# Optimization experiments

Measured on AMD Instinct MI355X. Metric: run time of the kernel, lower is better.

## Reference

```python
import jax, jax.numpy as jnp
import numpy as np

EPS = 1e-5

def layer_norm(h, g, b):
    m = h.mean(-1, keepdims=True)
    v = ((h - m) ** 2).mean(-1, keepdims=True)
    return (h - m) * jax.lax.rsqrt(v + EPS) * g + b

def setup_inputs() -> dict:
    key = jax.random.key(0)
    ks = jax.random.split(key, 16)
    B, D, C, H, EH, L = 64, 20000, 16, 64, 128, 32
    s = lambda k, fan_in, shape: jax.random.normal(k, shape, jnp.float32) / np.sqrt(fan_in)
    return {
        "x": jax.random.normal(ks[0], (B, D), jnp.float32),
        "mask": jax.random.randint(ks[1], (B, D), 0, 2, jnp.int32),
        "feature_embedding": jax.random.normal(ks[2], (D, C), jnp.float32),
        # h_layer: Linear(1+C -> H), LN, ReLU, Linear(H -> C), LN, ReLU
        "W1": s(ks[3], 1 + C, (1 + C, H)), "b1": jnp.zeros((H,), jnp.float32),
        "g1": jnp.ones((H,), jnp.float32), "be1": jnp.zeros((H,), jnp.float32),
        "W2": s(ks[4], H, (H, C)), "b2": jnp.zeros((C,), jnp.float32),
        "g2": jnp.ones((C,), jnp.float32), "be2": jnp.zeros((C,), jnp.float32),
        # encoder_mlp (FCLayers, 2 layers, LayerNorm + ReLU each): C -> EH -> 2L
        "We1": s(ks[5], C, (C, EH)), "bb1": jnp.zeros((EH,), jnp.float32),
        "gg1": jnp.ones((EH,), jnp.float32), "bbe1": jnp.zeros((EH,), jnp.float32),
        "We2": s(ks[6], EH, (EH, 2 * L)), "bb2": jnp.zeros((2 * L,), jnp.float32),
        "gg2": jnp.ones((2 * L,), jnp.float32), "bbe2": jnp.zeros((2 * L,), jnp.float32),
    }

def reference(x, mask, feature_embedding, W1, b1, g1, be1, W2, b2, g2, be2,
              We1, bb1, gg1, bbe1, We2, bb2, gg2, bbe2):
    B, D = x.shape
    C = feature_embedding.shape[1]
    # per-feature point-net: h_layer runs row-wise, so we compute it densely
    # for all (b, d) and zero out unobserved entries before pooling —
    # identical math to the per-sample masked gather in the original.
    h_in = jnp.concatenate(
        [x[..., None], jnp.broadcast_to(feature_embedding, (B, D, C))], axis=-1
    )  # [B, D, 1+C]
    h = jax.nn.relu(layer_norm(h_in @ W1 + b1, g1, be1))   # [B, D, H]
    h = jax.nn.relu(layer_norm(h @ W2 + b2, g2, be2))      # [B, D, C]
    m = mask.astype(h.dtype)
    summed = jnp.einsum('bdc,bd->bc', h, m)                # masked sum pool
    num_obs = jnp.maximum(m.sum(axis=1, keepdims=True), 1.0)
    c = summed / num_obs                                   # pool_mode='mean'
    # encoder_mlp
    e = jax.nn.relu(layer_norm(c @ We1 + bb1, gg1, bbe1))
    e = jax.nn.relu(layer_norm(e @ We2 + bb2, gg2, bbe2))  # [B, 2*latent]
    mu, logvar = jnp.split(e, 2, axis=-1)
    return mu, logvar
```

## Files before the change

### kernel.cpp

```cpp
#include <hip/hip_runtime.h>
#include <hip/hip_bf16.h>

#define EPSF 1e-5f

namespace {
constexpr int B = 64, D = 20000, C = 16, H = 64, EH = 128, L = 32;
constexpr int PB = 16;
constexpr int NB = 1024;
constexpr int MAXU = B * ((D + 63) / 64);
}

typedef __attribute__((ext_vector_type(8))) short bf16x8;
typedef __attribute__((ext_vector_type(4))) float f32x4;
typedef __attribute__((ext_vector_type(4))) unsigned int u32x4;

static __device__ __forceinline__ unsigned short f2bf(float f) {
    __hip_bfloat16 h = __float2bfloat16(f);
    return __builtin_bit_cast(unsigned short, h);
}
static __device__ __forceinline__ unsigned int packbf(float lo, float hi) {
    return ((unsigned int)f2bf(hi) << 16) | (unsigned int)f2bf(lo);
}

__global__ __launch_bounds__(1024) void k_prep(
    const int* __restrict__ mask, const float* __restrict__ fe,
    const float* __restrict__ W1, const float* __restrict__ b1,
    const float* __restrict__ W2,
    unsigned short* __restrict__ cd, int* __restrict__ cnt,
    unsigned short* __restrict__ febf,
    unsigned short* __restrict__ W1T, unsigned short* __restrict__ W2T)
{
    const int t = threadIdx.x;
    if (blockIdx.x < B) {
        const int b = blockIdx.x;
        const int lane = t & 63, wid = t >> 6;
        __shared__ int wc[16];
        const size_t bD = (size_t)b * D;
        constexpr int NIT = (D + 1023) / 1024;
        int mv = (t < D) ? mask[bD + t] : 0;
        int base = 0;
        for (int it = 0; it < NIT; ++it) {
            int mv_next = 0;
            const int dn = (it + 1) * 1024 + t;
            if (it + 1 < NIT && dn < D) mv_next = mask[bD + dn];
            const unsigned long long bal = __ballot(mv != 0);
            if (lane == 0) wc[wid] = __popcll(bal);
            __syncthreads();
            int woff = 0, tot = 0;
            #pragma unroll
            for (int k2 = 0; k2 < 16; ++k2) {
                const int c0 = wc[k2];
                tot += c0;
                if (k2 < wid) woff += c0;
            }
            if (mv) {
                const int d = it * 1024 + t;
                const int pre = __popcll(bal & ((1ull << lane) - 1ull));
                cd[bD + base + woff + pre] = (unsigned short)d;
            }
            base += tot;
            __syncthreads();
            mv = mv_next;
        }
        if (t == 0) cnt[b] = base;
    } else {
        const int pb = blockIdx.x - B;
        const int gtid = pb * 1024 + t;
        for (int u = gtid; u < (D * C) / 8; u += PB * 1024) {
            const float4 f0 = *(const float4*)(fe + (size_t)u * 8);
            const float4 f1 = *(const float4*)(fe + (size_t)u * 8 + 4);
            uint4 pk;
            pk.x = packbf(f0.x, f0.y); pk.y = packbf(f0.z, f0.w);
            pk.z = packbf(f1.x, f1.y); pk.w = packbf(f1.z, f1.w);
            *(uint4*)(febf + (size_t)u * 8) = pk;
        }
        if (pb == 0) {
            for (int e = t; e < H * 32; e += 1024) {
                const int rIdx = e >> 5, kk = e & 31;
                const int m = rIdx >> 4, rho = rIdx & 15;
                const int h = 32 * (m >> 1) + 8 * (rho >> 2) + 4 * (m & 1) + (rho & 3);
                float v = 0.f;
                if (kk < 16)       v = W1[(kk + 1) * H + h];
                else if (kk == 16) v = W1[h];
                else if (kk == 17) v = b1[h];
                W1T[e] = f2bf(v);
            }
        } else if (pb == 1) {
            for (int e = t; e < C * H; e += 1024) {
                const int c0 = e >> 6, hh = e & 63;
                W2T[e] = f2bf(W2[hh * C + c0]);
            }
        }
    }
}

__global__ __launch_bounds__(256, 4) void k_rows(
    const float* __restrict__ x, const unsigned short* __restrict__ cd,
    const int* __restrict__ cnt, const unsigned short* __restrict__ febf,
    const unsigned short* __restrict__ W1T, const unsigned short* __restrict__ W2T,
    const float* __restrict__ g1, const float* __restrict__ be1,
    const float* __restrict__ g2, const float* __restrict__ be2,
    const float* __restrict__ b2,
    float* __restrict__ part)
{
    const int tid = threadIdx.x;
    const int w = tid >> 6, lane = tid & 63;
    const int g = lane >> 4, q = lane & 15;

    const int cv  = cnt[lane];
    const int nuv = (cv + 63) >> 6;
    int Pi = nuv;
    #pragma unroll
    for (int off = 1; off < 64; off <<= 1) {
        const int pv = __shfl_up(Pi, off);
        if (lane >= off) Pi += pv;
    }
    const int T = __shfl(Pi, 63);

    bf16x8 w1f[4];
    #pragma unroll
    for (int m = 0; m < 4; ++m)
        w1f[m] = *(const bf16x8*)(W1T + (16 * m + q) * 32 + 8 * g);
    bf16x8 w2f[2];
    #pragma unroll
    for (int ks = 0; ks < 2; ++ks)
        w2f[ks] = *(const bf16x8*)(W2T + q * 64 + 32 * ks + 8 * g);

    float4 g1v[4], be1v[4];
    #pragma unroll
    for (int m = 0; m < 4; ++m) {
        const int h0 = 32 * (m >> 1) + 8 * g + 4 * (m & 1);
        g1v[m]  = *(const float4*)(g1  + h0);
        be1v[m] = *(const float4*)(be1 + h0);
    }
    const float4 g2v  = *(const float4*)(g2  + 4 * g);
    const float4 be2v = *(const float4*)(be2 + 4 * g);
    const float4 b2v  = *(const float4*)(b2  + 4 * g);

    const f32x4 z = {0.f, 0.f, 0.f, 0.f};

    for (int u = blockIdx.x * 4 + w; u < T; u += NB * 4) {
        const unsigned long long bl = __ballot(Pi <= u);
        const int b   = __popcll(bl);
        const int Pb  = __shfl(Pi, b);
        const int nub = __shfl(nuv, b);
        const int n   = __shfl(cv, b);
        const int base = (u - (Pb - nub)) * 64;
        const size_t bD = (size_t)b * D;

        const int idx  = base + lane;
        const int craw = (int)cd[bD + idx];
        const int dv   = (idx < n) ? craw : 0;

        bf16x8 hb[4];
        #pragma unroll
        for (int it = 0; it < 4; ++it) {
            const int dd = __shfl(dv, (it << 4) + q);
            bf16x8 hv;
            #pragma unroll
            for (int e = 0; e < 8; ++e) hv[e] = 0;
            if (g < 2) {
                hv = *(const bf16x8*)(febf + (size_t)dd * 16 + 8 * g);
            } else if (g == 2) {
                hv[0] = (short)f2bf(x[bD + dd]);
                hv[1] = (short)0x3F80;
            }
            hb[it] = hv;
        }

        f32x4 lacc = {0.f, 0.f, 0.f, 0.f};
        #pragma unroll
        for (int it = 0; it < 4; ++it) {
            const int gb = base + (it << 4);
            if (gb >= n) continue;
            f32x4 t1a[4];
            #pragma unroll
            for (int m = 0; m < 4; ++m)
                t1a[m] = __builtin_amdgcn_mfma_f32_16x16x32_bf16(w1f[m], hb[it], z, 0, 0, 0);

            float s0 = 0.f, s1 = 0.f, q0 = 0.f, q1 = 0.f;
            #pragma unroll
            for (int m = 0; m < 4; ++m) {
                s0 += t1a[m][0] + t1a[m][1];
                s1 += t1a[m][2] + t1a[m][3];
                q0 = fmaf(t1a[m][0], t1a[m][0], fmaf(t1a[m][1], t1a[m][1], q0));
                q1 = fmaf(t1a[m][2], t1a[m][2], fmaf(t1a[m][3], t1a[m][3], q1));
            }
            float s = s0 + s1, sq = q0 + q1;
            s  += __shfl_xor(s, 16);  sq += __shfl_xor(sq, 16);
            s  += __shfl_xor(s, 32);  sq += __shfl_xor(sq, 32);
            const float mean1 = s * (1.f / H);
            const float var1  = fmaxf(sq * (1.f / H) - mean1 * mean1, 0.f);
            const float rstd1 = rsqrtf(var1 + EPSF);

            unsigned int pw[8];
            #pragma unroll
            for (int m = 0; m < 4; ++m) {
                const float v0 = fmaxf(fmaf((t1a[m][0] - mean1) * rstd1, g1v[m].x, be1v[m].x), 0.f);
                const float v1 = fmaxf(fmaf((t1a[m][1] - mean1) * rstd1, g1v[m].y, be1v[m].y), 0.f);
                const float v2 = fmaxf(fmaf((t1a[m][2] - mean1) * rstd1, g1v[m].z, be1v[m].z), 0.f);
                const float v3 = fmaxf(fmaf((t1a[m][3] - mean1) * rstd1, g1v[m].w, be1v[m].w), 0.f);
                pw[2 * m]     = packbf(v0, v1);
                pw[2 * m + 1] = packbf(v2, v3);
            }
            const u32x4 r0 = {pw[0], pw[1], pw[2], pw[3]};
            const u32x4 r1 = {pw[4], pw[5], pw[6], pw[7]};
            const bf16x8 rb0 = __builtin_bit_cast(bf16x8, r0);
            const bf16x8 rb1 = __builtin_bit_cast(bf16x8, r1);

            f32x4 a2 = __builtin_amdgcn_mfma_f32_16x16x32_bf16(w2f[0], rb0, z, 0, 0, 0);
            a2 = __builtin_amdgcn_mfma_f32_16x16x32_bf16(w2f[1], rb1, a2, 0, 0, 0);
            a2[0] += b2v.x; a2[1] += b2v.y; a2[2] += b2v.z; a2[3] += b2v.w;

            float s2 = (a2[0] + a2[1]) + (a2[2] + a2[3]);
            float q2 = fmaf(a2[0], a2[0], fmaf(a2[1], a2[1],
                       fmaf(a2[2], a2[2], a2[3] * a2[3])));
            s2 += __shfl_xor(s2, 16);  q2 += __shfl_xor(q2, 16);
            s2 += __shfl_xor(s2, 32);  q2 += __shfl_xor(q2, 32);
            const float mean2 = s2 * (1.f / C);
            const float var2  = fmaxf(q2 * (1.f / C) - mean2 * mean2, 0.f);
            const float rstd2 = rsqrtf(var2 + EPSF);
            const float vm = (gb + q < n) ? 1.f : 0.f;
            lacc[0] += fmaxf(fmaf((a2[0] - mean2) * rstd2, g2v.x, be2v.x), 0.f) * vm;
            lacc[1] += fmaxf(fmaf((a2[1] - mean2) * rstd2, g2v.y, be2v.y), 0.f) * vm;
            lacc[2] += fmaxf(fmaf((a2[2] - mean2) * rstd2, g2v.z, be2v.z), 0.f) * vm;
            lacc[3] += fmaxf(fmaf((a2[3] - mean2) * rstd2, g2v.w, be2v.w), 0.f) * vm;
        }

        #pragma unroll
        for (int off = 1; off < 16; off <<= 1) {
            #pragma unroll
            for (int r = 0; r < 4; ++r) lacc[r] += __shfl_xor(lacc[r], off);
        }
        if (q == 0)
            *(float4*)(part + (size_t)u * C + 4 * g) =
                make_float4(lacc[0], lacc[1], lacc[2], lacc[3]);
    }
}

__global__ __launch_bounds__(EH) void k_enc(
    const float* __restrict__ part, const int* __restrict__ cnt,
    const float* __restrict__ We1, const float* __restrict__ bb1,
    const float* __restrict__ gg1, const float* __restrict__ bbe1,
    const float* __restrict__ We2, const float* __restrict__ bb2,
    const float* __restrict__ gg2, const float* __restrict__ bbe2,
    float* __restrict__ out)
{
    const int b = blockIdx.x;
    const int t = threadIdx.x;
    __shared__ int sP[64];
    __shared__ float red[8][16];
    __shared__ float cc[C];
    __shared__ float stats[2];
    __shared__ float buf[EH];
    __shared__ float buf2[2 * L];

    if (t < 64) {
        int p = (cnt[t] + 63) >> 6;
        #pragma unroll
        for (int off = 1; off < 64; off <<= 1) {
            const int pv = __shfl_up(p, off);
            if (t >= off) p += pv;
        }
        sP[t] = p;
    }
    __syncthreads();
    const int n = cnt[b];
    const int row0 = (b == 0) ? 0 : sP[b - 1];
    const int rows = sP[b] - row0;

    {
        const int c = t & 15, s = t >> 4;
        float ps = 0.f;
        for (int r = s; r < rows; r += 8)
            ps += part[(size_t)(row0 + r) * C + c];
        red[s][c] = ps;
    }
    __syncthreads();
    if (t < C) {
        float v = 0.f;
        #pragma unroll
        for (int s = 0; s < 8; ++s) v += red[s][t];
        cc[t] = v;
    }
    __syncthreads();
    const float inv = 1.f / fmaxf((float)n, 1.f);

    float v1 = bb1[t];
    #pragma unroll
    for (int c = 0; c < C; ++c)
        v1 = fmaf(cc[c] * inv, We1[c * EH + t], v1);
    buf[t] = v1;
    __syncthreads();
    if (t == 0) {
        float s = 0.f, ss = 0.f;
        for (int j2 = 0; j2 < EH; ++j2) { s += buf[j2]; ss = fmaf(buf[j2], buf[j2], ss); }
        float mn = s * (1.f / EH);
        float vr = fmaxf(ss * (1.f / EH) - mn * mn, 0.f);
        stats[0] = mn; stats[1] = rsqrtf(vr + EPSF);
    }
    __syncthreads();
    float e1 = fmaxf(fmaf((v1 - stats[0]) * stats[1], gg1[t], bbe1[t]), 0.f);
    __syncthreads();
    buf[t] = e1;
    __syncthreads();

    float v2 = 0.f;
    if (t < 2 * L) {
        v2 = bb2[t];
        #pragma unroll
        for (int h = 0; h < EH; ++h)
            v2 = fmaf(buf[h], We2[h * (2 * L) + t], v2);
        buf2[t] = v2;
    }
    __syncthreads();
    if (t == 0) {
        float s = 0.f, ss = 0.f;
        for (int j2 = 0; j2 < 2 * L; ++j2) { s += buf2[j2]; ss = fmaf(buf2[j2], buf2[j2], ss); }
        float mn = s * (1.f / (2 * L));
        float vr = fmaxf(ss * (1.f / (2 * L)) - mn * mn, 0.f);
        stats[0] = mn; stats[1] = rsqrtf(vr + EPSF);
    }
    __syncthreads();
    if (t < 2 * L) {
        float e2 = fmaxf(fmaf((v2 - stats[0]) * stats[1], gg2[t], bbe2[t]), 0.f);
        if (t < L) out[(size_t)b * L + t]                       = e2;
        else       out[(size_t)B * L + (size_t)b * L + (t - L)] = e2;
    }
}

extern "C" void kernel_launch(void* const* d_in, const int* in_sizes, int n_in,
                              void* d_out, int out_size, void* d_ws, size_t ws_size,
                              hipStream_t stream) {
    const float* x    = (const float*)d_in[0];
    const int*   mask = (const int*)d_in[1];
    const float* fe   = (const float*)d_in[2];
    const float* W1   = (const float*)d_in[3];
    const float* b1   = (const float*)d_in[4];
    const float* g1   = (const float*)d_in[5];
    const float* be1  = (const float*)d_in[6];
    const float* W2   = (const float*)d_in[7];
    const float* b2   = (const float*)d_in[8];
    const float* g2   = (const float*)d_in[9];
    const float* be2  = (const float*)d_in[10];
    const float* We1  = (const float*)d_in[11];
    const float* bb1  = (const float*)d_in[12];
    const float* gg1  = (const float*)d_in[13];
    const float* bbe1 = (const float*)d_in[14];
    const float* We2  = (const float*)d_in[15];
    const float* bb2  = (const float*)d_in[16];
    const float* gg2  = (const float*)d_in[17];
    const float* bbe2 = (const float*)d_in[18];
    float* out = (float*)d_out;

    char* wp = (char*)d_ws;
    float* part     = (float*)wp;               wp += (size_t)MAXU * C * 4;
    int*   cnt      = (int*)wp;                 wp += (size_t)B * 4;
    unsigned short* W1T  = (unsigned short*)wp; wp += (size_t)H * 32 * 2;
    unsigned short* W2T  = (unsigned short*)wp; wp += (size_t)C * H * 2;
    unsigned short* febf = (unsigned short*)wp; wp += (size_t)D * C * 2;
    unsigned short* cd   = (unsigned short*)wp;

    hipLaunchKernelGGL(k_prep, dim3(B + PB), dim3(1024), 0, stream,
                       mask, fe, W1, b1, W2, cd, cnt, febf, W1T, W2T);
    hipLaunchKernelGGL(k_rows, dim3(NB), dim3(256), 0, stream,
                       x, cd, cnt, febf, W1T, W2T, g1, be1, g2, be2, b2, part);
    hipLaunchKernelGGL(k_enc, dim3(B), dim3(EH), 0, stream,
                       part, cnt, We1, bb1, gg1, bbe1, We2, bb2, gg2, bbe2, out);
}
```

Measured before the change: 52.79 us.

## Materialize compacted per-sample bf16 feature rows in prep instead of index gather

The prep kernel now writes, for each observed (b, d), the bf16-packed feature embedding and a packed (x, 1) pair into a compacted per-sample buffer padded to 64 rows. The row kernel then reads these contiguously instead of gathering febf by index. This removes the index load, shuffle and dependent gather latency from the hot loop. In exchange it adds roughly 20 MB of extra HBM writes and reads, and that work sits on only 64 prep blocks. Separately, the row kernel's grid and occupancy hint are raised, bf16 packing uses the paired conversion intrinsic, and the per-chunk early-exit branch is dropped in favour of a mask.

```diff
diff --git a/kernel.cpp b/kernel.cpp
--- a/kernel.cpp
+++ b/kernel.cpp
@@ -5,8 +5,7 @@
 
 namespace {
 constexpr int B = 64, D = 20000, C = 16, H = 64, EH = 128, L = 32;
-constexpr int PB = 16;
-constexpr int NB = 1024;
+constexpr int NB = 1280;
 constexpr int MAXU = B * ((D + 63) / 64);
 }
 
@@ -21,13 +20,19 @@
 static __device__ __forceinline__ unsigned int packbf(float lo, float hi) {
     return ((unsigned int)f2bf(hi) << 16) | (unsigned int)f2bf(lo);
 }
+static __device__ __forceinline__ unsigned int cvtpk(float lo, float hi) {
+    __hip_bfloat162 h2 = __float22bfloat162_rn(make_float2(lo, hi));
+    return ((unsigned int)__builtin_bit_cast(unsigned short, h2.y) << 16)
+         | (unsigned int)__builtin_bit_cast(unsigned short, h2.x);
+}
 
 __global__ __launch_bounds__(1024) void k_prep(
-    const int* __restrict__ mask, const float* __restrict__ fe,
+    const int* __restrict__ mask, const float* __restrict__ x,
+    const float* __restrict__ fe,
     const float* __restrict__ W1, const float* __restrict__ b1,
     const float* __restrict__ W2,
-    unsigned short* __restrict__ cd, int* __restrict__ cnt,
-    unsigned short* __restrict__ febf,
+    int* __restrict__ cnt,
+    unsigned short* __restrict__ hfe, unsigned int* __restrict__ hxp,
     unsigned short* __restrict__ W1T, unsigned short* __restrict__ W2T)
 {
     const int t = threadIdx.x;
@@ -56,47 +61,53 @@
             if (mv) {
                 const int d = it * 1024 + t;
                 const int pre = __popcll(bal & ((1ull << lane) - 1ull));
-                cd[bD + base + woff + pre] = (unsigned short)d;
+                const int pos = base + woff + pre;
+                const float4 f0 = *(const float4*)(fe + (size_t)d * C);
+                const float4 f1 = *(const float4*)(fe + (size_t)d * C + 4);
+                const float4 f2 = *(const float4*)(fe + (size_t)d * C + 8);
+                const float4 f3 = *(const float4*)(fe + (size_t)d * C + 12);
+                uint4 p0, p1;
+                p0.x = packbf(f0.x, f0.y); p0.y = packbf(f0.z, f0.w);
+                p0.z = packbf(f1.x, f1.y); p0.w = packbf(f1.z, f1.w);
+                p1.x = packbf(f2.x, f2.y); p1.y = packbf(f2.z, f2.w);
+                p1.z = packbf(f3.x, f3.y); p1.w = packbf(f3.z, f3.w);
+                *(uint4*)(hfe + (bD + pos) * 16)     = p0;
+                *(uint4*)(hfe + (bD + pos) * 16 + 8) = p1;
+                hxp[bD + pos] = packbf(x[bD + d], 1.0f);
             }
             base += tot;
             __syncthreads();
             mv = mv_next;
         }
+        const int padend = (base + 63) & ~63;
+        for (int i = base + t; i < padend; i += 1024) {
+            *(uint4*)(hfe + (bD + i) * 16)     = make_uint4(0, 0, 0, 0);
+            *(uint4*)(hfe + (bD + i) * 16 + 8) = make_uint4(0, 0, 0, 0);
+            hxp[bD + i] = 0u;
+        }
         if (t == 0) cnt[b] = base;
+    } else if (blockIdx.x == B) {
+        for (int e = t; e < H * 32; e += 1024) {
+            const int rIdx = e >> 5, kk = e & 31;
+            const int m = rIdx >> 4, rho = rIdx & 15;
+            const int h = 32 * (m >> 1) + 8 * (rho >> 2) + 4 * (m & 1) + (rho & 3);
+            float v = 0.f;
+            if (kk < 16)       v = W1[(kk + 1) * H + h];
+            else if (kk == 16) v = W1[h];
+            else if (kk == 17) v = b1[h];
+            W1T[e] = f2bf(v);
+        }
     } else {
-        const int pb = blockIdx.x - B;
-        const int gtid = pb * 1024 + t;
-        for (int u = gtid; u < (D * C) / 8; u += PB * 1024) {
-            const float4 f0 = *(const float4*)(fe + (size_t)u * 8);
-            const float4 f1 = *(const float4*)(fe + (size_t)u * 8 + 4);
-            uint4 pk;
-            pk.x = packbf(f0.x, f0.y); pk.y = packbf(f0.z, f0.w);
-            pk.z = packbf(f1.x, f1.y); pk.w = packbf(f1.z, f1.w);
-            *(uint4*)(febf + (size_t)u * 8) = pk;
-        }
-        if (pb == 0) {
-            for (int e = t; e < H * 32; e += 1024) {
-                const int rIdx = e >> 5, kk = e & 31;
-                const int m = rIdx >> 4, rho = rIdx & 15;
-                const int h = 32 * (m >> 1) + 8 * (rho >> 2) + 4 * (m & 1) + (rho & 3);
-                float v = 0.f;
-                if (kk < 16)       v = W1[(kk + 1) * H + h];
-                else if (kk == 16) v = W1[h];
-                else if (kk == 17) v = b1[h];
-                W1T[e] = f2bf(v);
-            }
-        } else if (pb == 1) {
-            for (int e = t; e < C * H; e += 1024) {
-                const int c0 = e >> 6, hh = e & 63;
-                W2T[e] = f2bf(W2[hh * C + c0]);
-            }
-        }
-    }
-}
-
-__global__ __launch_bounds__(256, 4) void k_rows(
-    const float* __restrict__ x, const unsigned short* __restrict__ cd,
-    const int* __restrict__ cnt, const unsigned short* __restrict__ febf,
+        for (int e = t; e < C * H; e += 1024) {
+            const int c0 = e >> 6, hh = e & 63;
+            W2T[e] = f2bf(W2[hh * C + c0]);
+        }
+    }
+}
+
+__global__ __launch_bounds__(256, 5) void k_rows(
+    const int* __restrict__ cnt,
+    const unsigned short* __restrict__ hfe, const unsigned int* __restrict__ hxp,
     const unsigned short* __restrict__ W1T, const unsigned short* __restrict__ W2T,
     const float* __restrict__ g1, const float* __restrict__ be1,
     const float* __restrict__ g2, const float* __restrict__ be2,
@@ -146,24 +157,20 @@
         const int nub = __shfl(nuv, b);
         const int n   = __shfl(cv, b);
         const int base = (u - (Pb - nub)) * 64;
-        const size_t bD = (size_t)b * D;
-
-        const int idx  = base + lane;
-        const int craw = (int)cd[bD + idx];
-        const int dv   = (idx < n) ? craw : 0;
+        const size_t rowb = (size_t)b * D + base;
+        const int rem = n - base;
 
         bf16x8 hb[4];
         #pragma unroll
         for (int it = 0; it < 4; ++it) {
-            const int dd = __shfl(dv, (it << 4) + q);
-            bf16x8 hv;
-            #pragma unroll
-            for (int e = 0; e < 8; ++e) hv[e] = 0;
+            bf16x8 hv = {0, 0, 0, 0, 0, 0, 0, 0};
+            const int p = (it << 4) + q;
             if (g < 2) {
-                hv = *(const bf16x8*)(febf + (size_t)dd * 16 + 8 * g);
+                hv = *(const bf16x8*)(hfe + (rowb + p) * 16 + 8 * g);
             } else if (g == 2) {
-                hv[0] = (short)f2bf(x[bD + dd]);
-                hv[1] = (short)0x3F80;
+                const unsigned int xv = hxp[rowb + p];
+                const u32x4 tmp = {xv, 0u, 0u, 0u};
+                hv = __builtin_bit_cast(bf16x8, tmp);
             }
             hb[it] = hv;
         }
@@ -171,8 +178,6 @@
         f32x4 lacc = {0.f, 0.f, 0.f, 0.f};
         #pragma unroll
         for (int it = 0; it < 4; ++it) {
-            const int gb = base + (it << 4);
-            if (gb >= n) continue;
             f32x4 t1a[4];
             #pragma unroll
             for (int m = 0; m < 4; ++m)
@@ -200,8 +205,8 @@
                 const float v1 = fmaxf(fmaf((t1a[m][1] - mean1) * rstd1, g1v[m].y, be1v[m].y), 0.f);
                 const float v2 = fmaxf(fmaf((t1a[m][2] - mean1) * rstd1, g1v[m].z, be1v[m].z), 0.f);
                 const float v3 = fmaxf(fmaf((t1a[m][3] - mean1) * rstd1, g1v[m].w, be1v[m].w), 0.f);
-                pw[2 * m]     = packbf(v0, v1);
-                pw[2 * m + 1] = packbf(v2, v3);
+                pw[2 * m]     = cvtpk(v0, v1);
+                pw[2 * m + 1] = cvtpk(v2, v3);
             }
             const u32x4 r0 = {pw[0], pw[1], pw[2], pw[3]};
             const u32x4 r1 = {pw[4], pw[5], pw[6], pw[7]};
@@ -220,7 +225,7 @@
             const float mean2 = s2 * (1.f / C);
             const float var2  = fmaxf(q2 * (1.f / C) - mean2 * mean2, 0.f);
             const float rstd2 = rsqrtf(var2 + EPSF);
-            const float vm = (gb + q < n) ? 1.f : 0.f;
+            const float vm = ((it << 4) + q < rem) ? 1.f : 0.f;
             lacc[0] += fmaxf(fmaf((a2[0] - mean2) * rstd2, g2v.x, be2v.x), 0.f) * vm;
             lacc[1] += fmaxf(fmaf((a2[1] - mean2) * rstd2, g2v.y, be2v.y), 0.f) * vm;
             lacc[2] += fmaxf(fmaf((a2[2] - mean2) * rstd2, g2v.z, be2v.z), 0.f) * vm;
@@ -356,15 +361,15 @@
     char* wp = (char*)d_ws;
     float* part     = (float*)wp;               wp += (size_t)MAXU * C * 4;
     int*   cnt      = (int*)wp;                 wp += (size_t)B * 4;
-    unsigned short* W1T  = (unsigned short*)wp; wp += (size_t)H * 32 * 2;
-    unsigned short* W2T  = (unsigned short*)wp; wp += (size_t)C * H * 2;
-    unsigned short* febf = (unsigned short*)wp; wp += (size_t)D * C * 2;
-    unsigned short* cd   = (unsigned short*)wp;
-
-    hipLaunchKernelGGL(k_prep, dim3(B + PB), dim3(1024), 0, stream,
-                       mask, fe, W1, b1, W2, cd, cnt, febf, W1T, W2T);
+    unsigned short* W1T = (unsigned short*)wp;  wp += (size_t)H * 32 * 2;
+    unsigned short* W2T = (unsigned short*)wp;  wp += (size_t)C * H * 2;
+    unsigned int*   hxp = (unsigned int*)wp;    wp += (size_t)B * D * 4;
+    unsigned short* hfe = (unsigned short*)wp;
+
+    hipLaunchKernelGGL(k_prep, dim3(B + 2), dim3(1024), 0, stream,
+                       mask, x, fe, W1, b1, W2, cnt, hfe, hxp, W1T, W2T);
     hipLaunchKernelGGL(k_rows, dim3(NB), dim3(256), 0, stream,
-                       x, cd, cnt, febf, W1T, W2T, g1, be1, g2, be2, b2, part);
+                       cnt, hfe, hxp, W1T, W2T, g1, be1, g2, be2, b2, part);
     hipLaunchKernelGGL(k_enc, dim3(B), dim3(EH), 0, stream,
                        part, cnt, We1, bb1, gg1, bbe1, We2, bb2, gg2, bbe2, out);
 }
```

Result: slower. 119.3 us (+126.0%).
